# Kernel optimization log

Hardware: AMD Instinct MI355X
Metric: run time of the kernel (lower is better)

Reference implementation:

```python
import jax, jax.numpy as jnp
import numpy as np

N = 50000
E = 800000
IN_DIM = 128
HID = 128
HEADS = 8
OUT_DIM = 64
NEG_SLOPE = 0.2


def setup_inputs() -> dict:
    key = jax.random.key(0)
    ks = jax.random.split(key, 10)
    x = jax.random.normal(ks[0], (N, IN_DIM), dtype=jnp.float32)
    edge_index = jax.random.randint(ks[1], (2, E), 0, N, dtype=jnp.int64)
    c1 = HID // HEADS  # 16 per-head channels, layer 1
    # layer 1 params (GATConv: lin has no bias; att_src/att_dst are [1,H,C])
    W1 = jax.random.normal(ks[2], (IN_DIM, HEADS * c1), dtype=jnp.float32) * 0.1
    att_src1 = jax.random.normal(ks[3], (1, HEADS, c1), dtype=jnp.float32) * 0.1
    att_dst1 = jax.random.normal(ks[4], (1, HEADS, c1), dtype=jnp.float32) * 0.1
    b1 = jnp.zeros((HEADS * c1,), dtype=jnp.float32)  # concat=True -> bias size H*C
    # layer 2 params (heads=1, concat=False)
    W2 = jax.random.normal(ks[5], (HID, OUT_DIM), dtype=jnp.float32) * 0.1
    att_src2 = jax.random.normal(ks[6], (1, 1, OUT_DIM), dtype=jnp.float32) * 0.1
    att_dst2 = jax.random.normal(ks[7], (1, 1, OUT_DIM), dtype=jnp.float32) * 0.1
    b2 = jnp.zeros((OUT_DIM,), dtype=jnp.float32)
    return {"x": x, "edge_index": edge_index,
            "W1": W1, "att_src1": att_src1, "att_dst1": att_dst1, "b1": b1,
            "W2": W2, "att_src2": att_src2, "att_dst2": att_dst2, "b2": b2}


def _gat_conv(x, src, dst, W, att_src, att_dst, bias, heads, concat):
    n = x.shape[0]
    c = W.shape[1] // heads
    h = (x @ W).reshape(n, heads, c)                      # [N,H,C]
    a_src = jnp.sum(h * att_src, axis=-1)                 # [N,H]
    a_dst = jnp.sum(h * att_dst, axis=-1)                 # [N,H]
    e = a_src[src] + a_dst[dst]                           # [E,H]
    e = jnp.where(e > 0, e, NEG_SLOPE * e)                # leaky_relu
    # segment softmax over incoming edges of each dst node
    m = jax.ops.segment_max(e, dst, num_segments=n)       # [N,H]
    ex = jnp.exp(e - m[dst])
    denom = jax.ops.segment_sum(ex, dst, num_segments=n)  # [N,H]
    alpha = ex / (denom[dst] + 1e-16)                     # [E,H]
    msg = h[src] * alpha[:, :, None]                      # [E,H,C]
    out = jax.ops.segment_sum(msg, dst, num_segments=n)   # [N,H,C]
    out = out.reshape(n, heads * c) if concat else out.mean(axis=1)
    return out + bias


def reference(x, edge_index, W1, att_src1, att_dst1, b1, W2, att_src2, att_dst2, b2):
    # add self-loops (PyG GATConv default add_self_loops=True)
    loops = jnp.arange(N, dtype=edge_index.dtype)
    src = jnp.concatenate([edge_index[0], loops])
    dst = jnp.concatenate([edge_index[1], loops])
    h = _gat_conv(x, src, dst, W1, att_src1, att_dst1, b1, HEADS, True)
    h = jax.nn.elu(h)
    out = _gat_conv(h, src, dst, W2, att_src2, att_dst2, b2, 1, False)
    return jax.nn.log_softmax(out, axis=1)
```

## Files before the change

kernel.cpp:

```cpp
#include <hip/hip_runtime.h>
#include <math.h>

#define N_NODES 50000
#define E_EDGES 800000
#define ET      (E_EDGES + N_NODES)
#define IN_DIM  128
#define HID     128
#define HEADS   8
#define C1      16
#define OUT_DIM 64
#define NEG_SLOPE 0.2f
#define LOG2E   1.4426950408889634f

#define TILE    8192
#define NT      ((ET + TILE - 1) / TILE)
#define NB      ((N_NODES + 255) / 256)

#define PREP_BLOCKS 112
#define MEGA_A (NT + PREP_BLOCKS)
#define L1T_BLOCKS ((N_NODES + 63) / 64)
#define L1TA 391
#define L1TB (L1T_BLOCKS - L1TA)
#define FUSE_BLOCKS ((N_NODES + 15) / 16)

typedef unsigned int uint32;
typedef __attribute__((ext_vector_type(8))) short bf16x8;
typedef __attribute__((ext_vector_type(4))) float f32x4;
typedef __attribute__((ext_vector_type(2))) float f32x2;

static __device__ __forceinline__ unsigned short f2bf(float f) {
    uint32 u = __float_as_uint(f);
    u += 0x7FFFu + ((u >> 16) & 1u);
    return (unsigned short)(u >> 16);
}

static __device__ __forceinline__ unsigned char f2fp8(float f) {
    int pk = __builtin_amdgcn_cvt_pk_fp8_f32(f, f, 0, false);
    return (unsigned char)(pk & 0xFF);
}


__global__ __launch_bounds__(256) void prep_all(
        const int* __restrict__ dst, int* __restrict__ cnt,
        const float* __restrict__ W1, const float* __restrict__ as1,
        const float* __restrict__ ad1, const float* __restrict__ W2,
        const float* __restrict__ as2, const float* __restrict__ ad2,
        unsigned short* __restrict__ w1t, unsigned short* __restrict__ p1t,
        unsigned short* __restrict__ w2t, unsigned short* __restrict__ p2t) {
    __shared__ int hist[NB];
    int blk = blockIdx.x, t = threadIdx.x;
    if (blk < NT) {
        for (int b = t; b < NB; b += 256) hist[b] = 0;
        __syncthreads();
        int base = blk * TILE;
        #pragma unroll
        for (int it = 0; it < TILE / 256; ++it) {
            int i = base + it * 256 + t;
            if (i < ET) {
                int d = (i < E_EDGES) ? dst[i] : (i - E_EDGES);
                atomicAdd(&hist[d >> 8], 1);
            }
        }
        __syncthreads();
        for (int b = t; b < NB; b += 256) cnt[blk * NB + b] = hist[b];
    } else {
        int b = blk - NT;
        if (b < 64) {
            int i = b * 256 + t;
            int n = i >> 7, k = i & 127;
            w1t[n * IN_DIM + k] = f2bf(W1[k * HID + n]);
        } else if (b < 96) {
            int i = (b - 64) * 256 + t;
            int n = i >> 7, k = i & 127;
            w2t[n * HID + k] = f2bf(W2[k * OUT_DIM + n]);
        } else if (b < 104) {
            int i = (b - 96) * 256 + t;
            int j = i >> 7, k = i & 127;
            int hh = j & 7;
            const float* a = (j < 8) ? as1 : ad1;
            float acc = 0.f;
            #pragma unroll
            for (int c = 0; c < C1; ++c)
                acc = fmaf(W1[k * HID + hh * C1 + c], a[hh * C1 + c], acc);
            p1t[j * IN_DIM + k] = f2bf(acc * LOG2E);
        } else {
            int i = (b - 104) * 256 + t;
            int j = i >> 7, k = i & 127;
            if (j < 2) {
                const float* a = (j == 0) ? as2 : ad2;
                float acc = 0.f;
                #pragma unroll
                for (int c = 0; c < OUT_DIM; ++c)
                    acc = fmaf(W2[k * OUT_DIM + c], a[c], acc);
                p2t[j * HID + k] = f2bf(acc * LOG2E);
            } else {
                p2t[j * HID + k] = 0;
            }
        }
    }
}


static __device__ __forceinline__ void l1_transform_body(
        int bb, int t,
        const float* __restrict__ x, const unsigned short* __restrict__ w1t,
        const unsigned short* __restrict__ p1t, unsigned char* __restrict__ h1f,
        float* __restrict__ a_src, float* __restrict__ a_dst) {
    int w = t >> 6, lane = t & 63;
    int l15 = lane & 15, quad = lane >> 4;
    int n0 = bb * 64 + w * 16;
    int mrow = n0 + l15;
    int mload = (mrow < N_NODES) ? mrow : (N_NODES - 1);

    bf16x8 af[4];
    #pragma unroll
    for (int s = 0; s < 4; ++s) {
        const float* xr = &x[(size_t)mload * IN_DIM + s * 32 + quad * 8];
        float4 lo = *(const float4*)xr;
        float4 hi = *(const float4*)(xr + 4);
        bf16x8 v;
        v[0] = (short)f2bf(lo.x); v[1] = (short)f2bf(lo.y);
        v[2] = (short)f2bf(lo.z); v[3] = (short)f2bf(lo.w);
        v[4] = (short)f2bf(hi.x); v[5] = (short)f2bf(hi.y);
        v[6] = (short)f2bf(hi.z); v[7] = (short)f2bf(hi.w);
        af[s] = v;
    }

    #pragma unroll
    for (int tt = 0; tt < 9; ++tt) {
        const unsigned short* Brow = (tt < 8) ? &w1t[(tt * 16 + l15) * IN_DIM]
                                              : &p1t[l15 * IN_DIM];
        f32x4 acc = {0.f, 0.f, 0.f, 0.f};
        #pragma unroll
        for (int s = 0; s < 4; ++s) {
            bf16x8 bf = *(const bf16x8*)&Brow[s * 32 + quad * 8];
            acc = __builtin_amdgcn_mfma_f32_16x16x32_bf16(af[s], bf, acc, 0, 0, 0);
        }
        int nodeb = n0 + quad * 4;
        if (tt < 8) {
            int ch = tt * 16 + l15;
            #pragma unroll
            for (int r = 0; r < 4; ++r)
                if (nodeb + r < N_NODES)
                    h1f[(size_t)(nodeb + r) * HID + ch] = f2fp8(acc[r]);
        } else {
            #pragma unroll
            for (int r = 0; r < 4; ++r) {
                if (nodeb + r < N_NODES) {
                    if (l15 < 8) a_src[(nodeb + r) * HEADS + l15] = acc[r];
                    else         a_dst[(nodeb + r) * HEADS + (l15 - 8)] = acc[r];
                }
            }
        }
    }
}


__global__ __launch_bounds__(256) void scatter_l1ta(
        const int* __restrict__ src, const int* __restrict__ dst,
        const int* __restrict__ cnt, int* __restrict__ bucketStart,
        uint32* __restrict__ pairs,
        const float* __restrict__ x, const unsigned short* __restrict__ w1t,
        const unsigned short* __restrict__ p1t, unsigned char* __restrict__ h1f,
        float* __restrict__ a_src, float* __restrict__ a_dst) {
    __shared__ int lcur[NB];
    __shared__ int sscan[256];
    int t = threadIdx.x;
    if (blockIdx.x >= NT) {
        l1_transform_body(blockIdx.x - NT, t, x, w1t, p1t, h1f, a_src, a_dst);
        return;
    }
    int tile = blockIdx.x;

    int run = 0, total = 0;
    if (t < NB) {
        for (int k = 0; k < NT; ++k) {
            int c = cnt[k * NB + t];
            if (k < tile) run += c;
            total += c;
        }
    }
    sscan[t] = (t < NB) ? total : 0;
    __syncthreads();
    #pragma unroll
    for (int off = 1; off < 256; off <<= 1) {
        int add = (t >= off) ? sscan[t - off] : 0;
        __syncthreads();
        sscan[t] += add;
        __syncthreads();
    }
    int bstart = sscan[t] - total;
    if (t < NB) {
        lcur[t] = bstart + run;
        if (tile == 0) bucketStart[t] = bstart;
    }
    if (tile == 0 && t == 0) bucketStart[NB] = ET;
    __syncthreads();

    int base = tile * TILE;
    #pragma unroll
    for (int it = 0; it < TILE / 256; ++it) {
        int i = base + it * 256 + t;
        if (i < ET) {
            int s, d;
            if (i < E_EDGES) { s = src[i]; d = dst[i]; }
            else             { s = d = i - E_EDGES; }
            int pos = atomicAdd(&lcur[d >> 8], 1);
            pairs[pos] = ((uint32)s << 8) | (uint32)(d & 255);
        }
    }
}


__global__ __launch_bounds__(256) void bucket_l1tb(
        const uint32* __restrict__ pairs, const int* __restrict__ bucketStart,
        int* __restrict__ row_start, int* __restrict__ csr_src,
        const float* __restrict__ x, const unsigned short* __restrict__ w1t,
        const unsigned short* __restrict__ p1t, unsigned char* __restrict__ h1f,
        float* __restrict__ a_src, float* __restrict__ a_dst) {
    __shared__ int sdeg[256];
    __shared__ int sscan[256];
    int t = threadIdx.x;
    if (blockIdx.x >= NB) {
        l1_transform_body(blockIdx.x - NB + L1TA, t, x, w1t, p1t, h1f, a_src, a_dst);
        return;
    }
    int b = blockIdx.x;
    int beg = bucketStart[b], end = bucketStart[b + 1];
    sdeg[t] = 0;
    __syncthreads();
    for (int j = beg + t; j < end; j += 256)
        atomicAdd(&sdeg[pairs[j] & 255u], 1);
    __syncthreads();
    int v = sdeg[t];
    sscan[t] = v;
    __syncthreads();
    #pragma unroll
    for (int off = 1; off < 256; off <<= 1) {
        int add = (t >= off) ? sscan[t - off] : 0;
        __syncthreads();
        sscan[t] += add;
        __syncthreads();
    }
    int pos0 = beg + sscan[t] - v;
    int n = b * 256 + t;
    if (n < N_NODES) row_start[n] = pos0;
    if (b == 0 && t == 0) row_start[N_NODES] = ET;
    __syncthreads();
    sscan[t] = pos0;
    __syncthreads();
    for (int j = beg + t; j < end; j += 256) {
        uint32 p = pairs[j];
        int pos = atomicAdd(&sscan[p & 255u], 1);
        csr_src[pos] = (int)(p >> 8);
    }
}


__global__ __launch_bounds__(256, 4) void l1agg_l2t(
        const unsigned char* __restrict__ h1f, const float* __restrict__ a_src,
        const float* __restrict__ a_dst, const int* __restrict__ row_start,
        const int* __restrict__ csr_src, const float* __restrict__ b1,
        const unsigned short* __restrict__ w2t, const unsigned short* __restrict__ p2t,
        unsigned char* __restrict__ h2f, float* __restrict__ a_src2,
        float* __restrict__ a_dst2) {
    __shared__ unsigned short ha[16][128];
    __shared__ int sdeg16[16];
    __shared__ unsigned char perm[16];
    int t = threadIdx.x;
    int w = t >> 6;
    uint32 lane = t & 63;
    uint32 quarter = lane >> 4;
    uint32 lane16 = lane & 15;
    int n0blk = blockIdx.x * 16;

    if (t < 16) {
        int n = n0blk + t;
        int nc = (n < N_NODES) ? n : (N_NODES - 1);
        sdeg16[t] = row_start[nc + 1] - row_start[nc];
    }
    __syncthreads();
    if (t < 16) {
        int d = sdeg16[t];
        int r = 0;
        #pragma unroll
        for (int j = 0; j < 16; ++j) {
            int dj = sdeg16[j];
            r += (dj < d) || (dj == d && j < t);
        }
        perm[r] = (unsigned char)t;
    }
    __syncthreads();

    {
        uint32 c0 = lane16 * 8u;
        uint32 h = lane16 >> 1;
        int n_local = (int)perm[w * 4 + (int)quarter];
        int n = n0blk + n_local;
        int nc = (n < N_NODES) ? n : (N_NODES - 1);
        int beg = row_start[nc], end = row_start[nc + 1];
        int cnt = end - beg;
        int kmax = cnt;
        kmax = max(kmax, __shfl_xor(kmax, 16, 64));
        kmax = max(kmax, __shfl_xor(kmax, 32, 64));
        float adst = a_dst[nc * HEADS + h];
        float l = 0.f;
        float a0 = 0.f, a1 = 0.f, a2 = 0.f, a3 = 0.f;
        float a4 = 0.f, a5 = 0.f, a6 = 0.f, a7 = 0.f;

        auto edge = [&](float e0, uint2 u0, bool live) {
            float e = e0 + adst;
            e = fmaxf(e, NEG_SLOPE * e);
            e = live ? e : -10000.f;
            float p = exp2f(e);
            l += p;
            f32x2 f01 = __builtin_amdgcn_cvt_pk_f32_fp8((int)u0.x, false);
            f32x2 f23 = __builtin_amdgcn_cvt_pk_f32_fp8((int)u0.x, true);
            f32x2 f45 = __builtin_amdgcn_cvt_pk_f32_fp8((int)u0.y, false);
            f32x2 f67 = __builtin_amdgcn_cvt_pk_f32_fp8((int)u0.y, true);
            a0 = fmaf(p, f01[0], a0);
            a1 = fmaf(p, f01[1], a1);
            a2 = fmaf(p, f23[0], a2);
            a3 = fmaf(p, f23[1], a3);
            a4 = fmaf(p, f45[0], a4);
            a5 = fmaf(p, f45[1], a5);
            a6 = fmaf(p, f67[0], a6);
            a7 = fmaf(p, f67[1], a7);
        };

        int k = 0;
        uint32 ssn[8];
        if (k + 8 <= kmax) {
            #pragma unroll
            for (int q = 0; q < 8; ++q) {
                int j = beg + q;
                int jc = (j < end) ? j : (end - 1);
                ssn[q] = (uint32)csr_src[jc];
            }
        }
        for (; k + 8 <= kmax; k += 8) {
            uint32 ss[8]; float ee[8]; uint2 uu[8];
            #pragma unroll
            for (int q = 0; q < 8; ++q) ss[q] = ssn[q];
            #pragma unroll
            for (int q = 0; q < 8; ++q) ee[q] = a_src[ss[q] * 8u + h];
            #pragma unroll
            for (int q = 0; q < 8; ++q) uu[q] = *(const uint2*)&h1f[(ss[q] << 7) + c0];
            int kn = k + 8;
            if (kn + 8 <= kmax) {
                #pragma unroll
                for (int q = 0; q < 8; ++q) {
                    int j = beg + kn + q;
                    int jc = (j < end) ? j : (end - 1);
                    ssn[q] = (uint32)csr_src[jc];
                }
            }
            #pragma unroll
            for (int q = 0; q < 8; ++q) edge(ee[q], uu[q], k + q < cnt);
        }
        for (; k < kmax; k += 4) {
            uint32 ss[4]; float ee[4]; uint2 uu[4];
            #pragma unroll
            for (int q = 0; q < 4; ++q) {
                int j = beg + k + q;
                int jc = (j < end) ? j : (end - 1);
                ss[q] = (uint32)csr_src[jc];
            }
            #pragma unroll
            for (int q = 0; q < 4; ++q) ee[q] = a_src[ss[q] * 8u + h];
            #pragma unroll
            for (int q = 0; q < 4; ++q) uu[q] = *(const uint2*)&h1f[(ss[q] << 7) + c0];
            #pragma unroll
            for (int q = 0; q < 4; ++q) edge(ee[q], uu[q], k + q < cnt);
        }

        float inv = 1.f / (l + 1e-16f);
        float v0 = a0 * inv + b1[c0 + 0];
        float v1 = a1 * inv + b1[c0 + 1];
        float v2 = a2 * inv + b1[c0 + 2];
        float v3 = a3 * inv + b1[c0 + 3];
        float v4 = a4 * inv + b1[c0 + 4];
        float v5 = a5 * inv + b1[c0 + 5];
        float v6 = a6 * inv + b1[c0 + 6];
        float v7 = a7 * inv + b1[c0 + 7];
        v0 = v0 > 0.f ? v0 : (__expf(v0) - 1.f);
        v1 = v1 > 0.f ? v1 : (__expf(v1) - 1.f);
        v2 = v2 > 0.f ? v2 : (__expf(v2) - 1.f);
        v3 = v3 > 0.f ? v3 : (__expf(v3) - 1.f);
        v4 = v4 > 0.f ? v4 : (__expf(v4) - 1.f);
        v5 = v5 > 0.f ? v5 : (__expf(v5) - 1.f);
        v6 = v6 > 0.f ? v6 : (__expf(v6) - 1.f);
        v7 = v7 > 0.f ? v7 : (__expf(v7) - 1.f);
        uint4 packed;
        packed.x = (uint32)f2bf(v0) | ((uint32)f2bf(v1) << 16);
        packed.y = (uint32)f2bf(v2) | ((uint32)f2bf(v3) << 16);
        packed.z = (uint32)f2bf(v4) | ((uint32)f2bf(v5) << 16);
        packed.w = (uint32)f2bf(v6) | ((uint32)f2bf(v7) << 16);
        uint32 g = lane16 ^ ((uint32)n_local & 15u);
        *(uint4*)&ha[n_local][g * 8] = packed;
    }
    __syncthreads();

    {
        int l15 = (int)lane16, quad = (int)quarter;
        int n0 = n0blk;
        int nloc = l15;

        bf16x8 af[4];
        #pragma unroll
        for (int s = 0; s < 4; ++s) {
            uint32 g = (uint32)(s * 4 + quad) ^ (uint32)l15;
            af[s] = *(const bf16x8*)&ha[nloc][g * 8];
        }

        #pragma unroll
        for (int pass = 0; pass < 2; ++pass) {
            if (pass == 1 && w != 0) break;
            int tt = (pass == 0) ? w : 4;
            const unsigned short* Brow = (tt < 4) ? &w2t[(tt * 16 + l15) * HID]
                                                  : &p2t[l15 * HID];
            f32x4 acc = {0.f, 0.f, 0.f, 0.f};
            #pragma unroll
            for (int s = 0; s < 4; ++s) {
                bf16x8 bf = *(const bf16x8*)&Brow[s * 32 + quad * 8];
                acc = __builtin_amdgcn_mfma_f32_16x16x32_bf16(af[s], bf, acc, 0, 0, 0);
            }
            int nodeb = n0 + quad * 4;
            if (tt < 4) {
                int ch = tt * 16 + l15;
                #pragma unroll
                for (int r = 0; r < 4; ++r)
                    if (nodeb + r < N_NODES)
                        h2f[(size_t)(nodeb + r) * OUT_DIM + ch] = f2fp8(acc[r]);
            } else {
                #pragma unroll
                for (int r = 0; r < 4; ++r) {
                    if (nodeb + r < N_NODES) {
                        if (l15 == 0) a_src2[nodeb + r] = acc[r];
                        else if (l15 == 1) a_dst2[nodeb + r] = acc[r];
                    }
                }
            }
        }
    }
}


__global__ __launch_bounds__(256) void l2_aggregate(
        const unsigned char* __restrict__ h2f, const float* __restrict__ a_src2,
        const float* __restrict__ a_dst2, const int* __restrict__ row_start,
        const int* __restrict__ csr_src, const float* __restrict__ b2,
        float* __restrict__ out) {
    __shared__ int sdeg16[16];
    __shared__ int perm16[16];
    int t = threadIdx.x;
    int w = t >> 6;
    uint32 lane = t & 63;
    uint32 quarter = lane >> 4;
    uint32 lane16 = lane & 15;
    int nbase = blockIdx.x * 16;
    if (t < 16)
        sdeg16[t] = row_start[nbase + t + 1] - row_start[nbase + t];
    __syncthreads();
    if (t < 16) {
        int d = sdeg16[t];
        int r = 0;
        #pragma unroll
        for (int j = 0; j < 16; ++j) {
            int dj = sdeg16[j];
            r += (dj < d) || (dj == d && j < t);
        }
        perm16[r] = t;
    }
    __syncthreads();
    int n = nbase + perm16[w * 4 + (int)quarter];
    uint32 c0 = lane16 * 4u;
    int beg = row_start[n], end = row_start[n + 1];
    int cnt = end - beg;
    int kmax = cnt;
    kmax = max(kmax, __shfl_xor(kmax, 16, 64));
    kmax = max(kmax, __shfl_xor(kmax, 32, 64));
    float adst = a_dst2[n];
    float l = 0.f, a0 = 0.f, a1 = 0.f, a2 = 0.f, a3 = 0.f;

    auto edge2 = [&](float e0, uint32 u0, bool live) {
        float e = e0 + adst;
        e = fmaxf(e, NEG_SLOPE * e);
        e = live ? e : -10000.f;
        float p = exp2f(e);
        l += p;
        f32x2 f01 = __builtin_amdgcn_cvt_pk_f32_fp8((int)u0, false);
        f32x2 f23 = __builtin_amdgcn_cvt_pk_f32_fp8((int)u0, true);
        a0 = fmaf(p, f01[0], a0);
        a1 = fmaf(p, f01[1], a1);
        a2 = fmaf(p, f23[0], a2);
        a3 = fmaf(p, f23[1], a3);
    };

    int k = 0;
    uint32 ssn[8];
    if (k + 8 <= kmax) {
        #pragma unroll
        for (int q = 0; q < 8; ++q) {
            int j = beg + q;
            int jc = (j < end) ? j : (end - 1);
            ssn[q] = (uint32)csr_src[jc];
        }
    }
    for (; k + 8 <= kmax; k += 8) {
        uint32 ss[8]; float ee[8]; uint32 uu[8];
        #pragma unroll
        for (int q = 0; q < 8; ++q) ss[q] = ssn[q];
        #pragma unroll
        for (int q = 0; q < 8; ++q) ee[q] = a_src2[ss[q]];
        #pragma unroll
        for (int q = 0; q < 8; ++q) uu[q] = *(const uint32*)&h2f[(ss[q] << 6) + c0];
        int kn = k + 8;
        if (kn + 8 <= kmax) {
            #pragma unroll
            for (int q = 0; q < 8; ++q) {
                int j = beg + kn + q;
                int jc = (j < end) ? j : (end - 1);
                ssn[q] = (uint32)csr_src[jc];
            }
        }
        #pragma unroll
        for (int q = 0; q < 8; ++q) edge2(ee[q], uu[q], k + q < cnt);
    }
    for (; k < kmax; k += 4) {
        uint32 ss[4]; float ee[4]; uint32 uu[4];
        #pragma unroll
        for (int q = 0; q < 4; ++q) {
            int j = beg + k + q;
            int jc = (j < end) ? j : (end - 1);
            ss[q] = (uint32)csr_src[jc];
        }
        #pragma unroll
        for (int q = 0; q < 4; ++q) ee[q] = a_src2[ss[q]];
        #pragma unroll
        for (int q = 0; q < 4; ++q) uu[q] = *(const uint32*)&h2f[(ss[q] << 6) + c0];
        #pragma unroll
        for (int q = 0; q < 4; ++q) edge2(ee[q], uu[q], k + q < cnt);
    }

    float inv = 1.f / (l + 1e-16f);
    float o0 = a0 * inv + b2[c0 + 0];
    float o1 = a1 * inv + b2[c0 + 1];
    float o2 = a2 * inv + b2[c0 + 2];
    float o3 = a3 * inv + b2[c0 + 3];
    float mx = fmaxf(fmaxf(o0, o1), fmaxf(o2, o3));
    #pragma unroll
    for (int m = 8; m > 0; m >>= 1) mx = fmaxf(mx, __shfl_xor(mx, m, 16));
    float ex = __expf(o0 - mx) + __expf(o1 - mx) + __expf(o2 - mx) + __expf(o3 - mx);
    #pragma unroll
    for (int m = 8; m > 0; m >>= 1) ex += __shfl_xor(ex, m, 16);
    float lse = mx + __logf(ex);
    float4 o = make_float4(o0 - lse, o1 - lse, o2 - lse, o3 - lse);
    *(float4*)&out[(size_t)n * OUT_DIM + c0] = o;
}


extern "C" void kernel_launch(void* const* d_in, const int* in_sizes, int n_in,
                              void* d_out, int out_size, void* d_ws, size_t ws_size,
                              hipStream_t stream) {
    const float* x   = (const float*)d_in[0];
    const int*   ei  = (const int*)d_in[1];
    const float* W1  = (const float*)d_in[2];
    const float* as1 = (const float*)d_in[3];
    const float* ad1 = (const float*)d_in[4];
    const float* b1  = (const float*)d_in[5];
    const float* W2  = (const float*)d_in[6];
    const float* as2 = (const float*)d_in[7];
    const float* ad2 = (const float*)d_in[8];
    const float* b2  = (const float*)d_in[9];
    float* out = (float*)d_out;

    const int* src = ei;
    const int* dst = ei + E_EDGES;

    char* ws = (char*)d_ws;
    size_t off = 0;
    auto alloc = [&](size_t bytes) -> void* {
        void* p = ws + off;
        off += (bytes + 255) & ~size_t(255);
        return p;
    };
    unsigned char*  h1f    = (unsigned char*)alloc((size_t)N_NODES * HID);
    unsigned char*  h2f    = (unsigned char*)alloc((size_t)N_NODES * OUT_DIM);
    unsigned short* w1t    = (unsigned short*)alloc((size_t)HID * IN_DIM * 2);
    unsigned short* p1t    = (unsigned short*)alloc((size_t)16 * IN_DIM * 2);
    unsigned short* w2t    = (unsigned short*)alloc((size_t)OUT_DIM * HID * 2);
    unsigned short* p2t    = (unsigned short*)alloc((size_t)16 * HID * 2);
    float* a_src1    = (float*)alloc((size_t)N_NODES * HEADS * 4);
    float* a_dst1    = (float*)alloc((size_t)N_NODES * HEADS * 4);
    float* a_src2    = (float*)alloc((size_t)N_NODES * 4);
    float* a_dst2    = (float*)alloc((size_t)N_NODES * 4);
    int*   row_start = (int*)alloc((size_t)(N_NODES + 1) * 4);
    int*   csr_src   = (int*)alloc((size_t)ET * 4);
    uint32* pairs    = (uint32*)alloc((size_t)ET * 4);
    int*   cnt       = (int*)alloc((size_t)NB * NT * 4);
    int*   bucketStart = (int*)alloc((size_t)(NB + 1) * 4);

    prep_all<<<MEGA_A, 256, 0, stream>>>(dst, cnt, W1, as1, ad1,
                                         W2, as2, ad2, w1t, p1t, w2t, p2t);
    scatter_l1ta<<<NT + L1TA, 256, 0, stream>>>(src, dst, cnt, bucketStart, pairs,
                                                x, w1t, p1t, h1f, a_src1, a_dst1);
    bucket_l1tb<<<NB + L1TB, 256, 0, stream>>>(pairs, bucketStart, row_start, csr_src,
                                               x, w1t, p1t, h1f, a_src1, a_dst1);
    l1agg_l2t<<<FUSE_BLOCKS, 256, 0, stream>>>(h1f, a_src1, a_dst1, row_start, csr_src,
                                               b1, w2t, p2t, h2f, a_src2, a_dst2);
    l2_aggregate<<<FUSE_BLOCKS, 256, 0, stream>>>(h2f, a_src2, a_dst2, row_start,
                                                  csr_src, b2, out);
}
```

Before: 187.4 us.

## Widen per-lane channel slices in both GAT aggregation kernels with 16-byte gathers

Both aggregation kernels now give each lane 16 channels instead of 8 (layer 1) or 4 (layer 2). Each lane gathers features with one 16-byte load, so more destination nodes are handled per wave: 8 per wave in layer 1 (32 per block) and 16 per wave in layer 2 (64 per block). The intent is to cut redundant per-edge index, attention-score and exp work, and to issue fewer, wider gather instructions. In exchange each lane holds more accumulator registers, the per-wave max-degree padding spans more nodes, and the layer-2 MFMA stage gains an extra pass.

```diff
diff --git a/kernel.cpp b/kernel.cpp
--- a/kernel.cpp
+++ b/kernel.cpp
@@ -21,7 +21,8 @@
 #define L1T_BLOCKS ((N_NODES + 63) / 64)
 #define L1TA 391
 #define L1TB (L1T_BLOCKS - L1TA)
-#define FUSE_BLOCKS ((N_NODES + 15) / 16)
+#define FUSE_BLOCKS ((N_NODES + 31) / 32)
+#define L2_BLOCKS   ((N_NODES + 63) / 64)
 
 typedef unsigned int uint32;
 typedef __attribute__((ext_vector_type(8))) short bf16x8;
@@ -264,28 +265,30 @@
         const unsigned short* __restrict__ w2t, const unsigned short* __restrict__ p2t,
         unsigned char* __restrict__ h2f, float* __restrict__ a_src2,
         float* __restrict__ a_dst2) {
-    __shared__ unsigned short ha[16][128];
-    __shared__ int sdeg16[16];
-    __shared__ unsigned char perm[16];
+    __shared__ unsigned short ha[32][128];
+    __shared__ int sdeg32[32];
+    __shared__ unsigned char perm[32];
     int t = threadIdx.x;
     int w = t >> 6;
     uint32 lane = t & 63;
     uint32 quarter = lane >> 4;
     uint32 lane16 = lane & 15;
-    int n0blk = blockIdx.x * 16;
-
-    if (t < 16) {
+    uint32 oct = lane >> 3;
+    uint32 lane8 = lane & 7;
+    int n0blk = blockIdx.x * 32;
+
+    if (t < 32) {
         int n = n0blk + t;
         int nc = (n < N_NODES) ? n : (N_NODES - 1);
-        sdeg16[t] = row_start[nc + 1] - row_start[nc];
-    }
-    __syncthreads();
-    if (t < 16) {
-        int d = sdeg16[t];
+        sdeg32[t] = row_start[nc + 1] - row_start[nc];
+    }
+    __syncthreads();
+    if (t < 32) {
+        int d = sdeg32[t];
         int r = 0;
         #pragma unroll
-        for (int j = 0; j < 16; ++j) {
-            int dj = sdeg16[j];
+        for (int j = 0; j < 32; ++j) {
+            int dj = sdeg32[j];
             r += (dj < d) || (dj == d && j < t);
         }
         perm[r] = (unsigned char)t;
@@ -293,22 +296,24 @@
     __syncthreads();
 
     {
-        uint32 c0 = lane16 * 8u;
-        uint32 h = lane16 >> 1;
-        int n_local = (int)perm[w * 4 + (int)quarter];
+        uint32 c0 = lane8 * 16u;
+        uint32 h = lane8;
+        int n_local = (int)perm[w * 8 + (int)oct];
         int n = n0blk + n_local;
         int nc = (n < N_NODES) ? n : (N_NODES - 1);
         int beg = row_start[nc], end = row_start[nc + 1];
         int cnt = end - beg;
         int kmax = cnt;
+        kmax = max(kmax, __shfl_xor(kmax, 8, 64));
         kmax = max(kmax, __shfl_xor(kmax, 16, 64));
         kmax = max(kmax, __shfl_xor(kmax, 32, 64));
         float adst = a_dst[nc * HEADS + h];
         float l = 0.f;
-        float a0 = 0.f, a1 = 0.f, a2 = 0.f, a3 = 0.f;
-        float a4 = 0.f, a5 = 0.f, a6 = 0.f, a7 = 0.f;
-
-        auto edge = [&](float e0, uint2 u0, bool live) {
+        float acc[16];
+        #pragma unroll
+        for (int i = 0; i < 16; ++i) acc[i] = 0.f;
+
+        auto edge = [&](float e0, uint4 u0, bool live) {
             float e = e0 + adst;
             e = fmaxf(e, NEG_SLOPE * e);
             e = live ? e : -10000.f;
@@ -318,14 +323,26 @@
             f32x2 f23 = __builtin_amdgcn_cvt_pk_f32_fp8((int)u0.x, true);
             f32x2 f45 = __builtin_amdgcn_cvt_pk_f32_fp8((int)u0.y, false);
             f32x2 f67 = __builtin_amdgcn_cvt_pk_f32_fp8((int)u0.y, true);
-            a0 = fmaf(p, f01[0], a0);
-            a1 = fmaf(p, f01[1], a1);
-            a2 = fmaf(p, f23[0], a2);
-            a3 = fmaf(p, f23[1], a3);
-            a4 = fmaf(p, f45[0], a4);
-            a5 = fmaf(p, f45[1], a5);
-            a6 = fmaf(p, f67[0], a6);
-            a7 = fmaf(p, f67[1], a7);
+            f32x2 f89 = __builtin_amdgcn_cvt_pk_f32_fp8((int)u0.z, false);
+            f32x2 fab = __builtin_amdgcn_cvt_pk_f32_fp8((int)u0.z, true);
+            f32x2 fcd = __builtin_amdgcn_cvt_pk_f32_fp8((int)u0.w, false);
+            f32x2 fef = __builtin_amdgcn_cvt_pk_f32_fp8((int)u0.w, true);
+            acc[0]  = fmaf(p, f01[0], acc[0]);
+            acc[1]  = fmaf(p, f01[1], acc[1]);
+            acc[2]  = fmaf(p, f23[0], acc[2]);
+            acc[3]  = fmaf(p, f23[1], acc[3]);
+            acc[4]  = fmaf(p, f45[0], acc[4]);
+            acc[5]  = fmaf(p, f45[1], acc[5]);
+            acc[6]  = fmaf(p, f67[0], acc[6]);
+            acc[7]  = fmaf(p, f67[1], acc[7]);
+            acc[8]  = fmaf(p, f89[0], acc[8]);
+            acc[9]  = fmaf(p, f89[1], acc[9]);
+            acc[10] = fmaf(p, fab[0], acc[10]);
+            acc[11] = fmaf(p, fab[1], acc[11]);
+            acc[12] = fmaf(p, fcd[0], acc[12]);
+            acc[13] = fmaf(p, fcd[1], acc[13]);
+            acc[14] = fmaf(p, fef[0], acc[14]);
+            acc[15] = fmaf(p, fef[1], acc[15]);
         };
 
         int k = 0;
@@ -339,13 +356,13 @@
             }
         }
         for (; k + 8 <= kmax; k += 8) {
-            uint32 ss[8]; float ee[8]; uint2 uu[8];
+            uint32 ss[8]; float ee[8]; uint4 uu[8];
             #pragma unroll
             for (int q = 0; q < 8; ++q) ss[q] = ssn[q];
             #pragma unroll
             for (int q = 0; q < 8; ++q) ee[q] = a_src[ss[q] * 8u + h];
             #pragma unroll
-            for (int q = 0; q < 8; ++q) uu[q] = *(const uint2*)&h1f[(ss[q] << 7) + c0];
+            for (int q = 0; q < 8; ++q) uu[q] = *(const uint4*)&h1f[(ss[q] << 7) + c0];
             int kn = k + 8;
             if (kn + 8 <= kmax) {
                 #pragma unroll
@@ -359,7 +376,7 @@
             for (int q = 0; q < 8; ++q) edge(ee[q], uu[q], k + q < cnt);
         }
         for (; k < kmax; k += 4) {
-            uint32 ss[4]; float ee[4]; uint2 uu[4];
+            uint32 ss[4]; float ee[4]; uint4 uu[4];
             #pragma unroll
             for (int q = 0; q < 4; ++q) {
                 int j = beg + k + q;
@@ -369,54 +386,52 @@
             #pragma unroll
             for (int q = 0; q < 4; ++q) ee[q] = a_src[ss[q] * 8u + h];
             #pragma unroll
-            for (int q = 0; q < 4; ++q) uu[q] = *(const uint2*)&h1f[(ss[q] << 7) + c0];
+            for (int q = 0; q < 4; ++q) uu[q] = *(const uint4*)&h1f[(ss[q] << 7) + c0];
             #pragma unroll
             for (int q = 0; q < 4; ++q) edge(ee[q], uu[q], k + q < cnt);
         }
 
         float inv = 1.f / (l + 1e-16f);
-        float v0 = a0 * inv + b1[c0 + 0];
-        float v1 = a1 * inv + b1[c0 + 1];
-        float v2 = a2 * inv + b1[c0 + 2];
-        float v3 = a3 * inv + b1[c0 + 3];
-        float v4 = a4 * inv + b1[c0 + 4];
-        float v5 = a5 * inv + b1[c0 + 5];
-        float v6 = a6 * inv + b1[c0 + 6];
-        float v7 = a7 * inv + b1[c0 + 7];
-        v0 = v0 > 0.f ? v0 : (__expf(v0) - 1.f);
-        v1 = v1 > 0.f ? v1 : (__expf(v1) - 1.f);
-        v2 = v2 > 0.f ? v2 : (__expf(v2) - 1.f);
-        v3 = v3 > 0.f ? v3 : (__expf(v3) - 1.f);
-        v4 = v4 > 0.f ? v4 : (__expf(v4) - 1.f);
-        v5 = v5 > 0.f ? v5 : (__expf(v5) - 1.f);
-        v6 = v6 > 0.f ? v6 : (__expf(v6) - 1.f);
-        v7 = v7 > 0.f ? v7 : (__expf(v7) - 1.f);
-        uint4 packed;
-        packed.x = (uint32)f2bf(v0) | ((uint32)f2bf(v1) << 16);
-        packed.y = (uint32)f2bf(v2) | ((uint32)f2bf(v3) << 16);
-        packed.z = (uint32)f2bf(v4) | ((uint32)f2bf(v5) << 16);
-        packed.w = (uint32)f2bf(v6) | ((uint32)f2bf(v7) << 16);
-        uint32 g = lane16 ^ ((uint32)n_local & 15u);
-        *(uint4*)&ha[n_local][g * 8] = packed;
+        float v[16];
+        #pragma unroll
+        for (int i = 0; i < 16; ++i) {
+            float vi = acc[i] * inv + b1[c0 + i];
+            v[i] = vi > 0.f ? vi : (__expf(vi) - 1.f);
+        }
+        uint4 pk0, pk1;
+        pk0.x = (uint32)f2bf(v[0])  | ((uint32)f2bf(v[1])  << 16);
+        pk0.y = (uint32)f2bf(v[2])  | ((uint32)f2bf(v[3])  << 16);
+        pk0.z = (uint32)f2bf(v[4])  | ((uint32)f2bf(v[5])  << 16);
+        pk0.w = (uint32)f2bf(v[6])  | ((uint32)f2bf(v[7])  << 16);
+        pk1.x = (uint32)f2bf(v[8])  | ((uint32)f2bf(v[9])  << 16);
+        pk1.y = (uint32)f2bf(v[10]) | ((uint32)f2bf(v[11]) << 16);
+        pk1.z = (uint32)f2bf(v[12]) | ((uint32)f2bf(v[13]) << 16);
+        pk1.w = (uint32)f2bf(v[14]) | ((uint32)f2bf(v[15]) << 16);
+        uint32 rl = (uint32)n_local & 15u;
+        uint32 g0 = (2u * lane8 + 0u) ^ rl;
+        uint32 g1 = (2u * lane8 + 1u) ^ rl;
+        *(uint4*)&ha[n_local][g0 * 8] = pk0;
+        *(uint4*)&ha[n_local][g1 * 8] = pk1;
     }
     __syncthreads();
 
     {
         int l15 = (int)lane16, quad = (int)quarter;
-        int n0 = n0blk;
-        int nloc = l15;
-
-        bf16x8 af[4];
-        #pragma unroll
-        for (int s = 0; s < 4; ++s) {
-            uint32 g = (uint32)(s * 4 + quad) ^ (uint32)l15;
-            af[s] = *(const bf16x8*)&ha[nloc][g * 8];
-        }
-
-        #pragma unroll
-        for (int pass = 0; pass < 2; ++pass) {
-            if (pass == 1 && w != 0) break;
-            int tt = (pass == 0) ? w : 4;
+
+        #pragma unroll
+        for (int pass = 0; pass < 3; ++pass) {
+            int ti, tt;
+            if (pass < 2) { ti = pass; tt = w; }
+            else { if (w >= 2) break; ti = w; tt = 4; }
+
+            int nloc = ti * 16 + l15;
+            bf16x8 af[4];
+            #pragma unroll
+            for (int s = 0; s < 4; ++s) {
+                uint32 g = (uint32)(s * 4 + quad) ^ (uint32)l15;
+                af[s] = *(const bf16x8*)&ha[nloc][g * 8];
+            }
+
             const unsigned short* Brow = (tt < 4) ? &w2t[(tt * 16 + l15) * HID]
                                                   : &p2t[l15 * HID];
             f32x4 acc = {0.f, 0.f, 0.f, 0.f};
@@ -425,7 +440,7 @@
                 bf16x8 bf = *(const bf16x8*)&Brow[s * 32 + quad * 8];
                 acc = __builtin_amdgcn_mfma_f32_16x16x32_bf16(af[s], bf, acc, 0, 0, 0);
             }
-            int nodeb = n0 + quad * 4;
+            int nodeb = n0blk + ti * 16 + quad * 4;
             if (tt < 4) {
                 int ch = tt * 16 + l15;
                 #pragma unroll
@@ -451,50 +466,77 @@
         const float* __restrict__ a_dst2, const int* __restrict__ row_start,
         const int* __restrict__ csr_src, const float* __restrict__ b2,
         float* __restrict__ out) {
-    __shared__ int sdeg16[16];
-    __shared__ int perm16[16];
+    __shared__ int sdeg64[64];
+    __shared__ unsigned char perm[64];
     int t = threadIdx.x;
     int w = t >> 6;
     uint32 lane = t & 63;
-    uint32 quarter = lane >> 4;
-    uint32 lane16 = lane & 15;
-    int nbase = blockIdx.x * 16;
-    if (t < 16)
-        sdeg16[t] = row_start[nbase + t + 1] - row_start[nbase + t];
-    __syncthreads();
-    if (t < 16) {
-        int d = sdeg16[t];
+    uint32 lane4 = lane & 3;
+    uint32 nidx = lane >> 2;
+    int nbase = blockIdx.x * 64;
+    if (t < 64) {
+        int n = nbase + t;
+        int nc = (n < N_NODES) ? n : (N_NODES - 1);
+        sdeg64[t] = row_start[nc + 1] - row_start[nc];
+    }
+    __syncthreads();
+    if (t < 64) {
+        int d = sdeg64[t];
         int r = 0;
         #pragma unroll
-        for (int j = 0; j < 16; ++j) {
-            int dj = sdeg16[j];
+        for (int j = 0; j < 64; ++j) {
+            int dj = sdeg64[j];
             r += (dj < d) || (dj == d && j < t);
         }
-        perm16[r] = t;
-    }
-    __syncthreads();
-    int n = nbase + perm16[w * 4 + (int)quarter];
-    uint32 c0 = lane16 * 4u;
-    int beg = row_start[n], end = row_start[n + 1];
+        perm[r] = (unsigned char)t;
+    }
+    __syncthreads();
+    int n = nbase + (int)perm[w * 16 + (int)nidx];
+    int nc = (n < N_NODES) ? n : (N_NODES - 1);
+    uint32 c0 = lane4 * 16u;
+    int beg = row_start[nc], end = row_start[nc + 1];
     int cnt = end - beg;
     int kmax = cnt;
+    kmax = max(kmax, __shfl_xor(kmax, 4, 64));
+    kmax = max(kmax, __shfl_xor(kmax, 8, 64));
     kmax = max(kmax, __shfl_xor(kmax, 16, 64));
     kmax = max(kmax, __shfl_xor(kmax, 32, 64));
-    float adst = a_dst2[n];
-    float l = 0.f, a0 = 0.f, a1 = 0.f, a2 = 0.f, a3 = 0.f;
-
-    auto edge2 = [&](float e0, uint32 u0, bool live) {
+    float adst = a_dst2[nc];
+    float l = 0.f;
+    float acc[16];
+    #pragma unroll
+    for (int i = 0; i < 16; ++i) acc[i] = 0.f;
+
+    auto edge2 = [&](float e0, uint4 u0, bool live) {
         float e = e0 + adst;
         e = fmaxf(e, NEG_SLOPE * e);
         e = live ? e : -10000.f;
         float p = exp2f(e);
         l += p;
-        f32x2 f01 = __builtin_amdgcn_cvt_pk_f32_fp8((int)u0, false);
-        f32x2 f23 = __builtin_amdgcn_cvt_pk_f32_fp8((int)u0, true);
-        a0 = fmaf(p, f01[0], a0);
-        a1 = fmaf(p, f01[1], a1);
-        a2 = fmaf(p, f23[0], a2);
-        a3 = fmaf(p, f23[1], a3);
+        f32x2 f01 = __builtin_amdgcn_cvt_pk_f32_fp8((int)u0.x, false);
+        f32x2 f23 = __builtin_amdgcn_cvt_pk_f32_fp8((int)u0.x, true);
+        f32x2 f45 = __builtin_amdgcn_cvt_pk_f32_fp8((int)u0.y, false);
+        f32x2 f67 = __builtin_amdgcn_cvt_pk_f32_fp8((int)u0.y, true);
+        f32x2 f89 = __builtin_amdgcn_cvt_pk_f32_fp8((int)u0.z, false);
+        f32x2 fab = __builtin_amdgcn_cvt_pk_f32_fp8((int)u0.z, true);
+        f32x2 fcd = __builtin_amdgcn_cvt_pk_f32_fp8((int)u0.w, false);
+        f32x2 fef = __builtin_amdgcn_cvt_pk_f32_fp8((int)u0.w, true);
+        acc[0]  = fmaf(p, f01[0], acc[0]);
+        acc[1]  = fmaf(p, f01[1], acc[1]);
+        acc[2]  = fmaf(p, f23[0], acc[2]);
+        acc[3]  = fmaf(p, f23[1], acc[3]);
+        acc[4]  = fmaf(p, f45[0], acc[4]);
+        acc[5]  = fmaf(p, f45[1], acc[5]);
+        acc[6]  = fmaf(p, f67[0], acc[6]);
+        acc[7]  = fmaf(p, f67[1], acc[7]);
+        acc[8]  = fmaf(p, f89[0], acc[8]);
+        acc[9]  = fmaf(p, f89[1], acc[9]);
+        acc[10] = fmaf(p, fab[0], acc[10]);
+        acc[11] = fmaf(p, fab[1], acc[11]);
+        acc[12] = fmaf(p, fcd[0], acc[12]);
+        acc[13] = fmaf(p, fcd[1], acc[13]);
+        acc[14] = fmaf(p, fef[0], acc[14]);
+        acc[15] = fmaf(p, fef[1], acc[15]);
     };
 
     int k = 0;
@@ -508,13 +550,13 @@
         }
     }
     for (; k + 8 <= kmax; k += 8) {
-        uint32 ss[8]; float ee[8]; uint32 uu[8];
+        uint32 ss[8]; float ee[8]; uint4 uu[8];
         #pragma unroll
         for (int q = 0; q < 8; ++q) ss[q] = ssn[q];
         #pragma unroll
         for (int q = 0; q < 8; ++q) ee[q] = a_src2[ss[q]];
         #pragma unroll
-        for (int q = 0; q < 8; ++q) uu[q] = *(const uint32*)&h2f[(ss[q] << 6) + c0];
+        for (int q = 0; q < 8; ++q) uu[q] = *(const uint4*)&h2f[(ss[q] << 6) + c0];
         int kn = k + 8;
         if (kn + 8 <= kmax) {
             #pragma unroll
@@ -528,7 +570,7 @@
         for (int q = 0; q < 8; ++q) edge2(ee[q], uu[q], k + q < cnt);
     }
     for (; k < kmax; k += 4) {
-        uint32 ss[4]; float ee[4]; uint32 uu[4];
+        uint32 ss[4]; float ee[4]; uint4 uu[4];
         #pragma unroll
         for (int q = 0; q < 4; ++q) {
             int j = beg + k + q;
@@ -538,25 +580,34 @@
         #pragma unroll
         for (int q = 0; q < 4; ++q) ee[q] = a_src2[ss[q]];
         #pragma unroll
-        for (int q = 0; q < 4; ++q) uu[q] = *(const uint32*)&h2f[(ss[q] << 6) + c0];
+        for (int q = 0; q < 4; ++q) uu[q] = *(const uint4*)&h2f[(ss[q] << 6) + c0];
         #pragma unroll
         for (int q = 0; q < 4; ++q) edge2(ee[q], uu[q], k + q < cnt);
     }
 
     float inv = 1.f / (l + 1e-16f);
-    float o0 = a0 * inv + b2[c0 + 0];
-    float o1 = a1 * inv + b2[c0 + 1];
-    float o2 = a2 * inv + b2[c0 + 2];
-    float o3 = a3 * inv + b2[c0 + 3];
-    float mx = fmaxf(fmaxf(o0, o1), fmaxf(o2, o3));
-    #pragma unroll
-    for (int m = 8; m > 0; m >>= 1) mx = fmaxf(mx, __shfl_xor(mx, m, 16));
-    float ex = __expf(o0 - mx) + __expf(o1 - mx) + __expf(o2 - mx) + __expf(o3 - mx);
-    #pragma unroll
-    for (int m = 8; m > 0; m >>= 1) ex += __shfl_xor(ex, m, 16);
+    float o[16];
+    #pragma unroll
+    for (int i = 0; i < 16; ++i) o[i] = acc[i] * inv + b2[c0 + i];
+    float mx = o[0];
+    #pragma unroll
+    for (int i = 1; i < 16; ++i) mx = fmaxf(mx, o[i]);
+    mx = fmaxf(mx, __shfl_xor(mx, 1, 64));
+    mx = fmaxf(mx, __shfl_xor(mx, 2, 64));
+    float ex = 0.f;
+    #pragma unroll
+    for (int i = 0; i < 16; ++i) ex += __expf(o[i] - mx);
+    ex += __shfl_xor(ex, 1, 64);
+    ex += __shfl_xor(ex, 2, 64);
     float lse = mx + __logf(ex);
-    float4 o = make_float4(o0 - lse, o1 - lse, o2 - lse, o3 - lse);
-    *(float4*)&out[(size_t)n * OUT_DIM + c0] = o;
+    if (n < N_NODES) {
+        #pragma unroll
+        for (int j = 0; j < 4; ++j) {
+            float4 ov = make_float4(o[j*4+0] - lse, o[j*4+1] - lse,
+                                    o[j*4+2] - lse, o[j*4+3] - lse);
+            *(float4*)&out[(size_t)n * OUT_DIM + c0 + j * 4] = ov;
+        }
+    }
 }
 
 
@@ -609,6 +660,6 @@
                                                x, w1t, p1t, h1f, a_src1, a_dst1);
     l1agg_l2t<<<FUSE_BLOCKS, 256, 0, stream>>>(h1f, a_src1, a_dst1, row_start, csr_src,
                                                b1, w2t, p2t, h2f, a_src2, a_dst2);
-    l2_aggregate<<<FUSE_BLOCKS, 256, 0, stream>>>(h2f, a_src2, a_dst2, row_start,
-                                                  csr_src, b2, out);
-}
+    l2_aggregate<<<L2_BLOCKS, 256, 0, stream>>>(h2f, a_src2, a_dst2, row_start,
+                                                csr_src, b2, out);
+}
```

Result: slower. 258.7 us (+38.0%).
